# Kernel tuning notes

Measured on AMD Instinct MI355X. Metric: run time of the kernel, lower is better.

## Reference

```python
import jax, jax.numpy as jnp
import numpy as np
import math

D_MODEL = 1024
N_HEADS = 16
N_QUBITS = 8
HEAD_DIM = D_MODEL // N_HEADS
B, L = 2, 2048


def setup_inputs() -> dict:
    key = jax.random.key(0)
    ks = jax.random.split(key, 16)
    s = 0.02
    return {
        "query": jax.random.normal(ks[0], (B, L, D_MODEL), jnp.float32),
        "key_": jax.random.normal(ks[1], (B, L, D_MODEL), jnp.float32),
        "value": jax.random.normal(ks[2], (B, L, D_MODEL), jnp.float32),
        "Wq": jax.random.normal(ks[3], (D_MODEL, D_MODEL), jnp.float32) * s,
        "bq": jnp.zeros((D_MODEL,), jnp.float32),
        "Wk": jax.random.normal(ks[4], (D_MODEL, D_MODEL), jnp.float32) * s,
        "bk": jnp.zeros((D_MODEL,), jnp.float32),
        "Wv": jax.random.normal(ks[5], (D_MODEL, D_MODEL), jnp.float32) * s,
        "bv": jnp.zeros((D_MODEL,), jnp.float32),
        "Wo": jax.random.normal(ks[6], (D_MODEL, D_MODEL), jnp.float32) * s,
        "bo": jnp.zeros((D_MODEL,), jnp.float32),
        "Wf": jax.random.normal(ks[7], (HEAD_DIM, N_QUBITS), jnp.float32) * s,  # feature map weight (input->qubits)
        "bf": jnp.zeros((N_QUBITS,), jnp.float32),
        "quantum_weights": jax.random.normal(ks[8], (N_HEADS, N_QUBITS), jnp.float32) * 0.1,
        "entanglement_strength": jnp.asarray(0.5, jnp.float32),
    }


def _heads(x):
    # [B, L, D] -> [B, H, L, head_dim]
    b, l, _ = x.shape
    return x.reshape(b, l, N_HEADS, HEAD_DIM).transpose(0, 2, 1, 3)


def reference(query, key_, value, Wq, bq, Wk, bk, Wv, bv, Wo, bo, Wf, bf, quantum_weights, entanglement_strength):
    Qh = _heads(query @ Wq.T + bq)   # [B,H,L,d]
    Kh = _heads(key_ @ Wk.T + bk)
    Vh = _heads(value @ Wv.T + bv)

    classical = jnp.einsum("bhid,bhjd->bhij", Qh, Kh) / math.sqrt(HEAD_DIM)

    # quantum feature map: tanh(linear) -> [B,H,L,Q]
    qq = jnp.tanh(jnp.einsum("bhld,dq->bhlq", Qh, Wf) + bf)
    kq = jnp.tanh(jnp.einsum("bhld,dq->bhlq", Kh, Wf) + bf)

    # mean_q w_q*cos(qq_i - kq_j) == (1/Q)[(w*cos qq)@cos(kq)^T + (w*sin qq)@sin(kq)^T]
    w = jax.nn.sigmoid(quantum_weights)[None, :, None, :]  # [1,H,1,Q]
    quantum = (
        jnp.einsum("bhiq,bhjq->bhij", jnp.cos(qq) * w, jnp.cos(kq))
        + jnp.einsum("bhiq,bhjq->bhij", jnp.sin(qq) * w, jnp.sin(kq))
    ) / N_QUBITS
    ent = jax.nn.sigmoid(entanglement_strength)
    quantum = quantum * ent

    mix = ent  # same sigmoid(entanglement_strength) used as mixing weight
    combined = (1.0 - mix) * classical + mix * quantum

    attn = jax.nn.softmax(combined, axis=-1)  # [B,H,L,L]
    attended = jnp.einsum("bhij,bhjd->bhid", attn, Vh)
    attended = attended.transpose(0, 2, 1, 3).reshape(query.shape[0], query.shape[1], D_MODEL)
    output = attended @ Wo.T + bo
    return output, attn.mean(axis=1)
```

## Files before the change

### kernel.cpp

```cpp
#include <hip/hip_runtime.h>


typedef unsigned short u16;
typedef unsigned int u32;
typedef short v8s __attribute__((ext_vector_type(8)));
typedef float v4f __attribute__((ext_vector_type(4)));

static __device__ __forceinline__ float b2f(u16 h) {
  union { u32 u; float f; } a; a.u = ((u32)h) << 16; return a.f;
}
static __device__ __forceinline__ u16 f2b(float f) {
  union { float f; u32 u; } a; a.f = f;
  u32 u = a.u;
  u32 r = u + 0x7FFFu + ((u >> 16) & 1u);
  return (u16)(r >> 16);
}
static __device__ __forceinline__ v4f mfma16(v8s a, v8s b, v4f c) {
  return __builtin_amdgcn_mfma_f32_16x16x32_bf16(a, b, c, 0, 0, 0);
}
static __device__ __forceinline__ void gload16(const u16* g, u16* l) {
  __builtin_amdgcn_global_load_lds((const __attribute__((address_space(1))) u32*)g,
                                   (__attribute__((address_space(3))) u32*)l, 16, 0, 0);
}
static __device__ __forceinline__ float exp2fast(float x) {
  float r; asm("v_exp_f32 %0, %1" : "=v"(r) : "v"(x)); return r;
}
static __device__ __forceinline__ u32 cvtpk_bf16(float lo, float hi) {
  u32 r; asm("v_cvt_pk_bf16_f32 %0, %1, %2" : "=v"(r) : "v"(lo), "v"(hi)); return r;
}

__global__ __launch_bounds__(256) void k_f2b_all(const float* __restrict__ q, const float* __restrict__ k,
                                                 const float* __restrict__ v, const float* __restrict__ wq,
                                                 const float* __restrict__ wk, const float* __restrict__ wv,
                                                 const float* __restrict__ wo, u16* __restrict__ y) {
  int i = blockIdx.x * 256 + threadIdx.x;
  const float* src; int off;
  if (i < 1048576)      { src = q;  off = i; }
  else if (i < 2097152) { src = k;  off = i - 1048576; }
  else if (i < 3145728) { src = v;  off = i - 2097152; }
  else if (i < 3407872) { src = wq; off = i - 3145728; }
  else if (i < 3670016) { src = wk; off = i - 3407872; }
  else if (i < 3932160) { src = wv; off = i - 3670016; }
  else                  { src = wo; off = i - 3932160; }
  float4 val = ((const float4*)src)[off];
  union { u16 s[4]; uint2 u; } o;
  o.s[0] = f2b(val.x); o.s[1] = f2b(val.y); o.s[2] = f2b(val.z); o.s[3] = f2b(val.w);
  ((uint2*)y)[i] = o.u;
}

__global__ __launch_bounds__(256) void k_gemm128(
    const u16* __restrict__ A0, const u16* __restrict__ A1, const u16* __restrict__ A2,
    const u16* __restrict__ B0, const u16* __restrict__ B1, const u16* __restrict__ B2,
    const float* __restrict__ bias0, const float* __restrict__ bias1, const float* __restrict__ bias2,
    u16* __restrict__ O0, u16* __restrict__ O1, u16* __restrict__ O2t,
    float* __restrict__ Cf) {
  __shared__ __align__(16) u16 pool[18432];
  u16* As = pool;
  u16* Bs = pool + 8192;
  const int K = 1024, N = 1024;
  int t = threadIdx.x, w = t >> 6, lane = t & 63, quad = lane >> 4, l16 = lane & 15;
  int z = blockIdx.z;
  const u16* A = (z == 0) ? A0 : (z == 1) ? A1 : A2;
  const u16* Bm = (z == 0) ? B0 : (z == 1) ? B1 : B2;
  const float* bias = (z == 0) ? bias0 : (z == 1) ? bias1 : bias2;
  int n0 = blockIdx.x * 128, m0 = blockIdx.y * 128;

  int srow = lane >> 2, scol = (lane & 3) * 8;
  const u16* gp[8]; u16* lp[8];
#pragma unroll
  for (int qi = 0; qi < 8; ++qi) {
    int mat = qi >> 2, kk = (qi >> 1) & 1, g = w + (qi & 1) * 4;
    int row = g * 16 + srow;
    gp[qi] = (mat ? Bm + (size_t)(n0 + row) * K : A + (size_t)(m0 + row) * K) + kk * 32 + scol;
    lp[qi] = (mat ? Bs : As) + kk * 4096 + g * 512;
  }

  int mrow = (w >> 1) * 64, ncol = (w & 1) * 64;
  v4f zf = {0.f, 0.f, 0.f, 0.f};
  v4f acc[4][4];
#pragma unroll
  for (int mi = 0; mi < 4; ++mi)
#pragma unroll
    for (int ni = 0; ni < 4; ++ni) acc[mi][ni] = zf;

  for (int k0 = 0; k0 < K; k0 += 64) {
    __syncthreads();
#pragma unroll
    for (int qi = 0; qi < 8; ++qi) gload16(gp[qi] + k0, lp[qi]);
    __syncthreads();
#pragma unroll
    for (int kk = 0; kk < 2; ++kk) {
      v8s af[4], bfr[4];
#pragma unroll
      for (int x = 0; x < 4; ++x) {
        af[x] = *(const v8s*)&As[kk * 4096 + (mrow + x * 16 + l16) * 32 + quad * 8];
        bfr[x] = *(const v8s*)&Bs[kk * 4096 + (ncol + x * 16 + l16) * 32 + quad * 8];
      }
#pragma unroll
      for (int mi = 0; mi < 4; ++mi)
#pragma unroll
        for (int ni = 0; ni < 4; ++ni)
          acc[mi][ni] = mfma16(af[mi], bfr[ni], acc[mi][ni]);
    }
  }

  float bv[4];
#pragma unroll
  for (int ni = 0; ni < 4; ++ni) bv[ni] = bias[n0 + ncol + ni * 16 + l16];

  if (Cf) {
#pragma unroll
    for (int mi = 0; mi < 4; ++mi)
#pragma unroll
      for (int ni = 0; ni < 4; ++ni)
#pragma unroll
        for (int r = 0; r < 4; ++r)
          Cf[(size_t)(m0 + mrow + mi * 16 + quad * 4 + r) * N + n0 + ncol + ni * 16 + l16] =
              acc[mi][ni][r] + bv[ni];
  } else if (z != 2) {
    u16* O = z ? O1 : O0;
#pragma unroll
    for (int mi = 0; mi < 4; ++mi)
#pragma unroll
      for (int ni = 0; ni < 4; ++ni)
#pragma unroll
        for (int r = 0; r < 4; ++r)
          O[(size_t)(m0 + mrow + mi * 16 + quad * 4 + r) * N + n0 + ncol + ni * 16 + l16] =
              f2b(acc[mi][ni][r] + bv[ni]);
  } else {
    __syncthreads();
    u16* Ts = pool + w * 64 * 68;
#pragma unroll
    for (int mi = 0; mi < 4; ++mi)
#pragma unroll
      for (int ni = 0; ni < 4; ++ni)
#pragma unroll
        for (int r = 0; r < 4; ++r)
          Ts[(mi * 16 + quad * 4 + r) * 68 + ni * 16 + l16] = f2b(acc[mi][ni][r] + bv[ni]);
    int c = lane;
    union { uint4 u[8]; u16 s[64]; } cb;
#pragma unroll
    for (int e = 0; e < 64; ++e) cb.s[e] = Ts[e * 68 + c];
    int bb = m0 >> 11, ml = m0 & 2047;
    u16* dst = O2t + ((size_t)(bb * 1024 + n0 + ncol + c)) * 2048 + ml + mrow;
#pragma unroll
    for (int e = 0; e < 8; ++e) *(uint4*)(dst + e * 8) = cb.u[e];
  }
}

__global__ __launch_bounds__(256) void k_features(const u16* __restrict__ Qp, const u16* __restrict__ Kp,
                                                  const float* __restrict__ Wf, const float* __restrict__ bff,
                                                  const float* __restrict__ qw, const float* __restrict__ entp,
                                                  u16* __restrict__ Qaa, u16* __restrict__ Kaa) {
  int isK = blockIdx.y;
  const u16* P = isK ? Kp : Qp;
  u16* Out = isK ? Kaa : Qaa;
  int idx = blockIdx.x * 256 + threadIdx.x;
  int b = idx >> 15, h = (idx >> 11) & 15, l = idx & 2047;
  const u16* src = P + ((size_t)(b * 2048 + l)) * 1024 + h * 64;
  u16* dst = Out + (size_t)idx * 96;
  const float4* Wf4 = (const float4*)Wf;

  float x[64];
#pragma unroll
  for (int g = 0; g < 8; ++g) {
    union { uint4 u; u16 s[8]; } uu;
    uu.u = *(const uint4*)(src + g * 8);
#pragma unroll
    for (int e = 0; e < 8; ++e) x[g * 8 + e] = b2f(uu.s[e]);
  }
  float qv[8];
#pragma unroll
  for (int qq = 0; qq < 8; ++qq) qv[qq] = bff[qq];
#pragma unroll
  for (int d = 0; d < 64; ++d) {
    float4 wa = Wf4[d * 2], wb = Wf4[d * 2 + 1];
    float xd = x[d];
    qv[0] += xd * wa.x; qv[1] += xd * wa.y; qv[2] += xd * wa.z; qv[3] += xd * wa.w;
    qv[4] += xd * wb.x; qv[5] += xd * wb.y; qv[6] += xd * wb.z; qv[7] += xd * wb.w;
  }
  float cs[8], sn[8];
#pragma unroll
  for (int qq = 0; qq < 8; ++qq) {
    float e2 = __expf(2.f * qv[qq]);
    float th = 1.f - 2.f / (e2 + 1.f);
    __sincosf(th, &sn[qq], &cs[qq]);
  }
  float ent = 1.f / (1.f + __expf(-entp[0]));
  union { uint4 u; u16 s[8]; } pc, ps;
  if (!isK) {
#pragma unroll
    for (int g = 0; g < 8; ++g) *(uint4*)(dst + g * 8) = *(const uint4*)(src + g * 8);
#pragma unroll
    for (int qq = 0; qq < 8; ++qq) {
      float sw = 1.f / (1.f + __expf(-qw[h * 8 + qq]));
      pc.s[qq] = f2b(cs[qq] * sw);
      ps.s[qq] = f2b(sn[qq] * sw);
    }
  } else {
    const float LOG2E = 1.44269504088896f;
    float c1 = (1.f - ent) * 0.125f * LOG2E, c2 = ent * ent * 0.125f * LOG2E;
#pragma unroll
    for (int g = 0; g < 8; ++g) {
      union { uint4 u; u16 s[8]; } ob;
#pragma unroll
      for (int e = 0; e < 8; ++e) ob.s[e] = f2b(x[g * 8 + e] * c1);
      *(uint4*)(dst + g * 8) = ob.u;
    }
#pragma unroll
    for (int qq = 0; qq < 8; ++qq) {
      pc.s[qq] = f2b(cs[qq] * c2);
      ps.s[qq] = f2b(sn[qq] * c2);
    }
  }
  *(uint4*)(dst + 64) = pc.u;
  *(uint4*)(dst + 72) = ps.u;
  uint4 z4 = {0, 0, 0, 0};
  *(uint4*)(dst + 80) = z4;
  *(uint4*)(dst + 88) = z4;
}

__global__ __launch_bounds__(256) void k_flash(const u16* __restrict__ Qa, const u16* __restrict__ Ka,
                                               const u16* __restrict__ VtG, u16* __restrict__ At,
                                               float* __restrict__ lb) {
  __shared__ __align__(16) u16 Ks[2][64][104];
  __shared__ __align__(16) u16 Vs[2][64][72];
  __shared__ __align__(16) u16 Ps[4][2][16][72];

  int t = threadIdx.x, w = t >> 6, lane = t & 63, quad = lane >> 4, l16 = lane & 15;
  int bid = blockIdx.x;
  int sem = ((bid & 7) << 6) | (bid >> 3);
  int i0 = (sem & 15) << 7;
  int hb = sem >> 4;
  int h = hb & 15, b = hb >> 4;
  size_t qbase = ((size_t)(b * 16 + h)) * 2048 * 96;
  v8s aq[2][3];
#pragma unroll
  for (int i16 = 0; i16 < 2; ++i16) {
    const u16* Qrow = Qa + qbase + (size_t)(i0 + w * 32 + i16 * 16 + l16) * 96;
#pragma unroll
    for (int ks = 0; ks < 3; ++ks) aq[i16][ks] = *(const v8s*)(Qrow + ks * 32 + quad * 8);
  }
  const u16* Kbase = Ka + qbase;
  const u16* Vbase = VtG + ((size_t)(b * 1024 + h * 64)) * 2048;

  const u16* kg[3]; int kdo[3];
#pragma unroll
  for (int p = 0; p < 3; ++p) {
    int idx = t + p * 256, r_ = idx / 12, c_ = idx % 12;
    kg[p] = Kbase + (size_t)r_ * 96 + c_ * 8;
    kdo[p] = r_ * 104 + c_ * 8;
  }
  u16* ks0 = &Ks[0][0][0];
  u16* ks1 = &Ks[1][0][0];

  const u16* vg0 = Vbase + (size_t)(t >> 3) * 2048 + (t & 7) * 8;
  const u16* vg1 = vg0 + (size_t)32 * 2048;
  u16* vsb = &Vs[0][0][0];
  int vdo0 = (t >> 3) * 72 + (t & 7) * 8;
  int vdo1 = vdo0 + 32 * 72;
  const int VSTRIDE = 64 * 72;

  v4f zf = {0.f, 0.f, 0.f, 0.f};
  v4f oacc[2][4];
#pragma unroll
  for (int i16 = 0; i16 < 2; ++i16)
#pragma unroll
    for (int d16 = 0; d16 < 4; ++d16) oacc[i16][d16] = zf;
  float l_acc[2] = {0.f, 0.f};

  uint4 fk0 = *(const uint4*)kg[0];
  uint4 fk1 = *(const uint4*)kg[1];
  uint4 fk2 = *(const uint4*)kg[2];
  kg[0] += 6144; kg[1] += 6144; kg[2] += 6144;
  *(uint4*)(ks0 + kdo[0]) = fk0;
  *(uint4*)(ks0 + kdo[1]) = fk1;
  *(uint4*)(ks0 + kdo[2]) = fk2;
  fk0 = *(const uint4*)kg[0];
  fk1 = *(const uint4*)kg[1];
  fk2 = *(const uint4*)kg[2];
  kg[0] += 6144; kg[1] += 6144; kg[2] += 6144;
  uint4 va0 = *(const uint4*)vg0;
  uint4 va1 = *(const uint4*)vg1;
  *(uint4*)(vsb + vdo0) = va0;
  *(uint4*)(vsb + vdo1) = va1;
  __syncthreads();

  for (int j0 = 0; j0 < 2048; j0 += 64) {
    int cur = (j0 >> 6) & 1;
    const u16* kb = cur ? ks1 : ks0;
    u16* kw = cur ? ks0 : ks1;
    const u16* vcur = vsb + cur * VSTRIDE;
    bool more = (j0 + 64) < 2048;
    if (more) {
      *(uint4*)(kw + kdo[0]) = fk0;
      *(uint4*)(kw + kdo[1]) = fk1;
      *(uint4*)(kw + kdo[2]) = fk2;
    }
    if (j0 + 128 < 2048) {
      fk0 = *(const uint4*)kg[0];
      fk1 = *(const uint4*)kg[1];
      fk2 = *(const uint4*)kg[2];
      kg[0] += 6144; kg[1] += 6144; kg[2] += 6144;
    }
    if (more) {
      va0 = *(const uint4*)(vg0 + j0 + 64);
      va1 = *(const uint4*)(vg1 + j0 + 64);
    }

    v4f sacc[2][4];
#pragma unroll
    for (int i16 = 0; i16 < 2; ++i16)
#pragma unroll
      for (int j16 = 0; j16 < 4; ++j16) sacc[i16][j16] = zf;
    __builtin_amdgcn_s_setprio(1);
#pragma unroll
    for (int j16 = 0; j16 < 4; ++j16)
#pragma unroll
      for (int ks = 0; ks < 3; ++ks) {
        v8s kf = *(const v8s*)(kb + (j16 * 16 + l16) * 104 + ks * 32 + quad * 8);
        sacc[0][j16] = mfma16(kf, aq[0][ks], sacc[0][j16]);
        sacc[1][j16] = mfma16(kf, aq[1][ks], sacc[1][j16]);
      }
    __builtin_amdgcn_s_setprio(0);

#pragma unroll
    for (int i16 = 0; i16 < 2; ++i16)
#pragma unroll
      for (int j16 = 0; j16 < 4; ++j16) {
        float e0 = exp2fast(sacc[i16][j16][0]);
        float e1 = exp2fast(sacc[i16][j16][1]);
        float e2 = exp2fast(sacc[i16][j16][2]);
        float e3 = exp2fast(sacc[i16][j16][3]);
        l_acc[i16] += (e0 + e1) + (e2 + e3);
        uint2 pp;
        pp.x = cvtpk_bf16(e0, e1);
        pp.y = cvtpk_bf16(e2, e3);
        *(uint2*)&Ps[w][i16][l16][j16 * 16 + quad * 4] = pp;
      }

    __builtin_amdgcn_s_setprio(1);
#pragma unroll
    for (int jh = 0; jh < 2; ++jh) {
      v8s pf0 = *(const v8s*)&Ps[w][0][l16][jh * 32 + quad * 8];
      v8s pf1 = *(const v8s*)&Ps[w][1][l16][jh * 32 + quad * 8];
#pragma unroll
      for (int d16 = 0; d16 < 4; ++d16) {
        v8s vv = *(const v8s*)(vcur + (d16 * 16 + l16) * 72 + jh * 32 + quad * 8);
        oacc[0][d16] = mfma16(pf0, vv, oacc[0][d16]);
        oacc[1][d16] = mfma16(pf1, vv, oacc[1][d16]);
      }
    }
    __builtin_amdgcn_s_setprio(0);
    if (more) {
      u16* vwr = vsb + (cur ^ 1) * VSTRIDE;
      *(uint4*)(vwr + vdo0) = va0;
      *(uint4*)(vwr + vdo1) = va1;
      __syncthreads();
    }
  }

#pragma unroll
  for (int i16 = 0; i16 < 2; ++i16) {
    l_acc[i16] += __shfl_xor(l_acc[i16], 16, 64);
    l_acc[i16] += __shfl_xor(l_acc[i16], 32, 64);
    float linv = 1.f / l_acc[i16];
#pragma unroll
    for (int r = 0; r < 4; ++r) {
      float li = __shfl(linv, quad * 4 + r, 64);
      int ri = i0 + w * 32 + i16 * 16 + quad * 4 + r;
#pragma unroll
      for (int d16 = 0; d16 < 4; ++d16)
        At[((size_t)(b * 2048 + ri)) * 1024 + h * 64 + d16 * 16 + l16] = f2b(oacc[i16][d16][r] * li);
    }
    if (lane < 16) {
      size_t mbase = ((size_t)(b * 16 + h)) * 2048;
      lb[mbase + i0 + w * 32 + i16 * 16 + lane] = l_acc[i16];
    }
  }
}

__global__ __launch_bounds__(256) void k_pass2(const u16* __restrict__ Qa, const u16* __restrict__ Ka,
                                               const float* __restrict__ lb,
                                               float* __restrict__ out1) {
  __shared__ __align__(16) u16 Ks[64][104];
  __shared__ float Ls[16][128];
  int t = threadIdx.x, w = t >> 6, lane = t & 63, quad = lane >> 4, l16 = lane & 15;
  int bid = blockIdx.x;
  int sem = ((bid & 7) << 7) | (bid >> 3);
  int xcd = sem >> 7;
  int b = xcd >> 2;
  int i0 = ((((xcd & 3) << 2) | (sem & 3))) << 7;
  int j0 = ((sem >> 2) & 31) << 6;

#pragma unroll
  for (int rep = 0; rep < 8; ++rep) {
    int idx = t + rep * 256;
    int hh = idx >> 7, il = idx & 127;
    Ls[hh][il] = 0.0625f / lb[((size_t)(b * 16 + hh)) * 2048 + i0 + il];
  }

  size_t base0 = (size_t)b * 16 * 2048 * 96;
  const u16* kg[3]; u16* kd[3];
#pragma unroll
  for (int rep = 0; rep < 3; ++rep) {
    int idx = t + rep * 256;
    int r_ = idx / 12, c_ = idx % 12;
    kg[rep] = Ka + base0 + (size_t)(j0 + r_) * 96 + c_ * 8;
    kd[rep] = &Ks[r_][c_ * 8];
  }
  uint4 f0 = *(const uint4*)kg[0];
  uint4 f1 = *(const uint4*)kg[1];
  uint4 f2 = *(const uint4*)kg[2];

  const u16* q0 = Qa + base0 + (size_t)(i0 + w * 32 + l16) * 96 + quad * 8;
  const u16* q1 = q0 + 16 * 96;

  v4f zf = {0.f, 0.f, 0.f, 0.f};
  v4f macc[2][4];
#pragma unroll
  for (int i16 = 0; i16 < 2; ++i16)
#pragma unroll
    for (int j16 = 0; j16 < 4; ++j16) macc[i16][j16] = zf;

  v8s a[2][3];
#pragma unroll
  for (int ks = 0; ks < 3; ++ks) {
    a[0][ks] = *(const v8s*)(q0 + ks * 32);
    a[1][ks] = *(const v8s*)(q1 + ks * 32);
  }

  for (int h = 0; h < 16; ++h) {
    *(uint4*)kd[0] = f0;
    *(uint4*)kd[1] = f1;
    *(uint4*)kd[2] = f2;
    __syncthreads();
    if (h < 15) {
      kg[0] += 196608; kg[1] += 196608; kg[2] += 196608;
      f0 = *(const uint4*)kg[0];
      f1 = *(const uint4*)kg[1];
      f2 = *(const uint4*)kg[2];
    }

    v4f sacc[2][4];
#pragma unroll
    for (int i16 = 0; i16 < 2; ++i16)
#pragma unroll
      for (int j16 = 0; j16 < 4; ++j16) sacc[i16][j16] = zf;
#pragma unroll
    for (int ks = 0; ks < 3; ++ks)
#pragma unroll
      for (int j16 = 0; j16 < 4; ++j16) {
        v8s kf = *(const v8s*)&Ks[j16 * 16 + l16][ks * 32 + quad * 8];
        sacc[0][j16] = mfma16(a[0][ks], kf, sacc[0][j16]);
        sacc[1][j16] = mfma16(a[1][ks], kf, sacc[1][j16]);
      }

    if (h < 15) {
      q0 += 196608; q1 += 196608;
#pragma unroll
      for (int ks = 0; ks < 3; ++ks) {
        a[0][ks] = *(const v8s*)(q0 + ks * 32);
        a[1][ks] = *(const v8s*)(q1 + ks * 32);
      }
    }

    float li[2][4];
#pragma unroll
    for (int i16 = 0; i16 < 2; ++i16)
#pragma unroll
      for (int r = 0; r < 4; ++r)
        li[i16][r] = Ls[h][w * 32 + i16 * 16 + quad * 4 + r];
#pragma unroll
    for (int i16 = 0; i16 < 2; ++i16)
#pragma unroll
      for (int j16 = 0; j16 < 4; ++j16)
#pragma unroll
        for (int r = 0; r < 4; ++r)
          macc[i16][j16][r] += exp2fast(sacc[i16][j16][r]) * li[i16][r];
    __syncthreads();
  }

  float* o = out1 + (size_t)b * 2048 * 2048;
#pragma unroll
  for (int i16 = 0; i16 < 2; ++i16)
#pragma unroll
    for (int j16 = 0; j16 < 4; ++j16)
#pragma unroll
      for (int r = 0; r < 4; ++r)
        o[(size_t)(i0 + w * 32 + i16 * 16 + quad * 4 + r) * 2048 + j0 + j16 * 16 + l16] =
            macc[i16][j16][r];
}

extern "C" void kernel_launch(void* const* d_in, const int* in_sizes, int n_in,
                              void* d_out, int out_size, void* d_ws, size_t ws_size,
                              hipStream_t stream) {
  (void)in_sizes; (void)n_in; (void)out_size; (void)ws_size;
  const float* query = (const float*)d_in[0];
  const float* key_  = (const float*)d_in[1];
  const float* value = (const float*)d_in[2];
  const float* Wq = (const float*)d_in[3];
  const float* bq = (const float*)d_in[4];
  const float* Wk = (const float*)d_in[5];
  const float* bk = (const float*)d_in[6];
  const float* Wv = (const float*)d_in[7];
  const float* bv = (const float*)d_in[8];
  const float* Wo = (const float*)d_in[9];
  const float* bo = (const float*)d_in[10];
  const float* Wf = (const float*)d_in[11];
  const float* bff = (const float*)d_in[12];
  const float* qw = (const float*)d_in[13];
  const float* entp = (const float*)d_in[14];

  char* p = (char*)d_ws;
  u16* Xq  = (u16*)(p + 0);
  u16* Xk  = (u16*)(p + 8388608);
  u16* Xv  = (u16*)(p + 16777216);
  u16* Wqb = (u16*)(p + 25165824);
  u16* Wkb = (u16*)(p + 27262976);
  u16* Wvb = (u16*)(p + 29360128);
  u16* Qp  = (u16*)(p + 33554432);
  u16* Kp  = (u16*)(p + 41943040);
  u16* VtG = (u16*)(p + 50331648);
  u16* Qaa = (u16*)(p + 58720256);
  u16* Kaa = (u16*)(p + 71303168);
  float* lb = (float*)(p + 84148224);
  u16* At  = (u16*)(p + 84410368);
  u16* Wob = (u16*)(p + 31457280);

  k_f2b_all<<<16384, 256, 0, stream>>>(query, key_, value, Wq, Wk, Wv, Wo, Xq);

  k_gemm128<<<dim3(8, 32, 3), 256, 0, stream>>>(Xq, Xk, Xv, Wqb, Wkb, Wvb, bq, bk, bv,
                                                Qp, Kp, VtG, nullptr);

  k_features<<<dim3(256, 2), 256, 0, stream>>>(Qp, Kp, Wf, bff, qw, entp, Qaa, Kaa);

  k_flash<<<dim3(512), 256, 0, stream>>>(Qaa, Kaa, VtG, At, lb);

  k_pass2<<<dim3(1024), 256, 0, stream>>>(Qaa, Kaa, lb, (float*)d_out + 4194304);

  k_gemm128<<<dim3(8, 32, 1), 256, 0, stream>>>(At, At, At, Wob, Wob, Wob, bo, bo, bo,
                                                nullptr, nullptr, nullptr, (float*)d_out);
}
```

Before: 330.8 us.

## Swizzle V tile in LDS, hoist V fragments, double-buffer K in pass2

```diff
diff --git a/kernel.cpp b/kernel.cpp
--- a/kernel.cpp
+++ b/kernel.cpp
@@ -224,8 +224,8 @@
                                                const u16* __restrict__ VtG, u16* __restrict__ At,
                                                float* __restrict__ lb) {
   __shared__ __align__(16) u16 Ks[2][64][104];
-  __shared__ __align__(16) u16 Vs[2][64][72];
-  __shared__ __align__(16) u16 Ps[4][2][16][72];
+  __shared__ __align__(16) u16 Vs[2][4096];
+  __shared__ __align__(16) u16 Ps[4][16][72];
 
   int t = threadIdx.x, w = t >> 6, lane = t & 63, quad = lane >> 4, l16 = lane & 15;
   int bid = blockIdx.x;
@@ -254,12 +254,15 @@
   u16* ks0 = &Ks[0][0][0];
   u16* ks1 = &Ks[1][0][0];
 
-  const u16* vg0 = Vbase + (size_t)(t >> 3) * 2048 + (t & 7) * 8;
+  {
+  }
+  int vrow = t >> 3, vunit = t & 7;
+  const u16* vg0 = Vbase + (size_t)vrow * 2048 + vunit * 8;
   const u16* vg1 = vg0 + (size_t)32 * 2048;
-  u16* vsb = &Vs[0][0][0];
-  int vdo0 = (t >> 3) * 72 + (t & 7) * 8;
-  int vdo1 = vdo0 + 32 * 72;
-  const int VSTRIDE = 64 * 72;
+  int vdo0 = vrow * 64 + (vunit ^ (vrow & 7)) * 8;
+  int vdo1 = vdo0 + 32 * 64;
+  u16* vsb = &Vs[0][0];
+  const int VSTRIDE = 4096;
 
   v4f zf = {0.f, 0.f, 0.f, 0.f};
   v4f oacc[2][4];
@@ -268,6 +271,7 @@
 #pragma unroll
     for (int d16 = 0; d16 < 4; ++d16) oacc[i16][d16] = zf;
   float l_acc[2] = {0.f, 0.f};
+  int lsw = l16 & 7;
 
   uint4 fk0 = *(const uint4*)kg[0];
   uint4 fk1 = *(const uint4*)kg[1];
@@ -324,8 +328,16 @@
       }
     __builtin_amdgcn_s_setprio(0);
 
-#pragma unroll
-    for (int i16 = 0; i16 < 2; ++i16)
+    v8s vf[8];
+#pragma unroll
+    for (int d16 = 0; d16 < 4; ++d16)
+#pragma unroll
+      for (int jh = 0; jh < 2; ++jh)
+        vf[d16 * 2 + jh] =
+            *(const v8s*)(vcur + (d16 * 16 + l16) * 64 + ((jh * 4 + quad) ^ lsw) * 8);
+
+#pragma unroll
+    for (int i16 = 0; i16 < 2; ++i16) {
 #pragma unroll
       for (int j16 = 0; j16 < 4; ++j16) {
         float e0 = exp2fast(sacc[i16][j16][0]);
@@ -336,22 +348,19 @@
         uint2 pp;
         pp.x = cvtpk_bf16(e0, e1);
         pp.y = cvtpk_bf16(e2, e3);
-        *(uint2*)&Ps[w][i16][l16][j16 * 16 + quad * 4] = pp;
+        *(uint2*)&Ps[w][l16][j16 * 16 + quad * 4] = pp;
       }
-
-    __builtin_amdgcn_s_setprio(1);
-#pragma unroll
-    for (int jh = 0; jh < 2; ++jh) {
-      v8s pf0 = *(const v8s*)&Ps[w][0][l16][jh * 32 + quad * 8];
-      v8s pf1 = *(const v8s*)&Ps[w][1][l16][jh * 32 + quad * 8];
-#pragma unroll
-      for (int d16 = 0; d16 < 4; ++d16) {
-        v8s vv = *(const v8s*)(vcur + (d16 * 16 + l16) * 72 + jh * 32 + quad * 8);
-        oacc[0][d16] = mfma16(pf0, vv, oacc[0][d16]);
-        oacc[1][d16] = mfma16(pf1, vv, oacc[1][d16]);
+      __builtin_amdgcn_s_setprio(1);
+#pragma unroll
+      for (int jh = 0; jh < 2; ++jh) {
+        v8s pf = *(const v8s*)&Ps[w][l16][jh * 32 + quad * 8];
+#pragma unroll
+        for (int d16 = 0; d16 < 4; ++d16)
+          oacc[i16][d16] = mfma16(pf, vf[d16 * 2 + jh], oacc[i16][d16]);
       }
-    }
-    __builtin_amdgcn_s_setprio(0);
+      __builtin_amdgcn_s_setprio(0);
+    }
+
     if (more) {
       u16* vwr = vsb + (cur ^ 1) * VSTRIDE;
       *(uint4*)(vwr + vdo0) = va0;
@@ -383,7 +392,7 @@
 __global__ __launch_bounds__(256) void k_pass2(const u16* __restrict__ Qa, const u16* __restrict__ Ka,
                                                const float* __restrict__ lb,
                                                float* __restrict__ out1) {
-  __shared__ __align__(16) u16 Ks[64][104];
+  __shared__ __align__(16) u16 Ks[2][64][104];
   __shared__ float Ls[16][128];
   int t = threadIdx.x, w = t >> 6, lane = t & 63, quad = lane >> 4, l16 = lane & 15;
   int bid = blockIdx.x;
@@ -407,11 +416,16 @@
     int idx = t + rep * 256;
     int r_ = idx / 12, c_ = idx % 12;
     kg[rep] = Ka + base0 + (size_t)(j0 + r_) * 96 + c_ * 8;
-    kd[rep] = &Ks[r_][c_ * 8];
-  }
+    kd[rep] = &Ks[0][r_][c_ * 8];
+  }
+  const int KSTRIDE = 64 * 104;
+
   uint4 f0 = *(const uint4*)kg[0];
   uint4 f1 = *(const uint4*)kg[1];
   uint4 f2 = *(const uint4*)kg[2];
+  *(uint4*)kd[0] = f0; *(uint4*)kd[1] = f1; *(uint4*)kd[2] = f2;
+  kg[0] += 196608; kg[1] += 196608; kg[2] += 196608;
+  f0 = *(const uint4*)kg[0]; f1 = *(const uint4*)kg[1]; f2 = *(const uint4*)kg[2];
 
   const u16* q0 = Qa + base0 + (size_t)(i0 + w * 32 + l16) * 96 + quad * 8;
   const u16* q1 = q0 + 16 * 96;
@@ -429,18 +443,20 @@
     a[0][ks] = *(const v8s*)(q0 + ks * 32);
     a[1][ks] = *(const v8s*)(q1 + ks * 32);
   }
+  __syncthreads();
 
   for (int h = 0; h < 16; ++h) {
-    *(uint4*)kd[0] = f0;
-    *(uint4*)kd[1] = f1;
-    *(uint4*)kd[2] = f2;
-    __syncthreads();
     if (h < 15) {
+      int aoff = ((h & 1) ^ 1) * KSTRIDE;
+      *(uint4*)(kd[0] + aoff) = f0;
+      *(uint4*)(kd[1] + aoff) = f1;
+      *(uint4*)(kd[2] + aoff) = f2;
+    }
+    if (h < 14) {
       kg[0] += 196608; kg[1] += 196608; kg[2] += 196608;
-      f0 = *(const uint4*)kg[0];
-      f1 = *(const uint4*)kg[1];
-      f2 = *(const uint4*)kg[2];
-    }
+      f0 = *(const uint4*)kg[0]; f1 = *(const uint4*)kg[1]; f2 = *(const uint4*)kg[2];
+    }
+    const u16* Kb = &Ks[h & 1][0][0];
 
     v4f sacc[2][4];
 #pragma unroll
@@ -451,7 +467,7 @@
     for (int ks = 0; ks < 3; ++ks)
 #pragma unroll
       for (int j16 = 0; j16 < 4; ++j16) {
-        v8s kf = *(const v8s*)&Ks[j16 * 16 + l16][ks * 32 + quad * 8];
+        v8s kf = *(const v8s*)(Kb + (j16 * 16 + l16) * 104 + ks * 32 + quad * 8);
         sacc[0][j16] = mfma16(a[0][ks], kf, sacc[0][j16]);
         sacc[1][j16] = mfma16(a[1][ks], kf, sacc[1][j16]);
       }
```

Result: no change. 330.2 us (-0.2%).
